# Performance work log

Hardware: AMD Instinct MI355X
Metric: run time of the kernel (lower is better)

The kernel has to match this reference:

```python
import jax, jax.numpy as jnp
import numpy as np

B, N, INNER, OUT, DEPTH = 128, 128, 40, 512, 2
F = INNER + 1  # last channel is the bond/adjacency channel


def setup_inputs() -> dict:
    key = jax.random.key(0)
    k0, k1, k2, k3, k4 = jax.random.split(key, 5)
    return {
        "graph": jax.random.normal(k0, (B, N, N, F), dtype=jnp.float32),
        # build() inits: identity tiled for W_inner, uniform*0.05 for W_output, zero biases.
        # We add small noise so the reference exercises nondegenerate paths.
        "W_inner": jnp.tile(jnp.eye(INNER, dtype=jnp.float32)[None], (DEPTH + 1, 1, 1))
        + 0.05 * jax.random.normal(k1, (DEPTH + 1, INNER, INNER), dtype=jnp.float32),
        "b_inner": 0.05 * jax.random.normal(k2, (DEPTH + 1, 1, INNER), dtype=jnp.float32),
        "W_output": 0.05 * jax.random.normal(k3, (DEPTH + 1, INNER, OUT), dtype=jnp.float32),
        "b_output": 0.05 * jax.random.normal(k4, (DEPTH + 1, 1, OUT), dtype=jnp.float32),
    }


def reference(graph, W_inner, b_inner, W_output, b_output):
    depth = W_inner.shape[0] - 1

    def fp_contrib(attrs, d):
        # softmax over fingerprint dim, summed over atoms -> (OUT,)
        logits = attrs[:, :-1] @ W_output[d] + b_output[d, 0]
        return jax.nn.softmax(logits, axis=-1).sum(axis=0)

    def single(g):  # g: (N, N, F) for one molecule
        n = g.shape[0]
        # attributes[i, f] = g[i, i, f]  (per-atom diagonal extraction)
        attrs = jnp.diagonal(g, axis1=0, axis2=1).T  # (N, F)
        bonds = g[:, :, -1]                          # (N, N)
        boa = bonds + jnp.eye(n, dtype=g.dtype)      # bonds_or_atoms
        fp = fp_contrib(attrs, 0)
        cur = g
        for d in range(1, depth + 1):
            # sum over neighbors j: pre[i, f] = sum_j cur[i, j, f], drop bond channel
            pre = cur[:, :, :-1].sum(axis=1)                     # (N, INNER)
            new_core = pre @ W_inner[d] + b_inner[d, 0]          # linear inner activation
            new_attrs = jnp.concatenate([new_core, attrs[:, -1:]], axis=1)  # (N, F)
            # new_graph[i,j,f] = cur[i,j,f] + boa[j,i] * (new_attrs[i,f] - attrs[i,f])
            cur = cur + boa.T[:, :, None] * (new_attrs - attrs)[:, None, :]
            attrs = new_attrs
            fp = fp + fp_contrib(attrs, d)
        return fp  # (OUT,)

    return jax.vmap(single)(graph)  # (B, OUT)
```

## Files before the change

### kernel.cpp

```cpp
#include <hip/hip_runtime.h>

#define Bn 128
#define Nn 128
#define Fn 41
#define INNERn 40
#define OUTn 512
#define SLAB (Nn*Fn)

__global__ __launch_bounds__(256) void k1_reduce(
    const float* __restrict__ g, float* __restrict__ X0,
    float* __restrict__ pre1, float* __restrict__ S)
{
    __shared__ float lds[SLAB];
    __shared__ float part[6*INNERn];
    const int t = threadIdx.x;
    const int blk = blockIdx.x;
    const int b = blk >> 7;
    const int i = blk & 127;

    if (t < 40) {
        X0[(size_t)blk*INNERn + t] = g[(size_t)blk*SLAB + i*Fn + t];
    }

    const float4* __restrict__ src = (const float4*)(g + (size_t)blk * SLAB);
    float4* dst = (float4*)lds;
    #pragma unroll
    for (int it = 0; it < 5; ++it) dst[t + 256*it] = src[t + 256*it];
    if (t < (SLAB/4 - 1280)) dst[1280 + t] = src[1280 + t];
    __syncthreads();

    if (t < 240) {
        const int grp = t / 40;
        const int f = t - grp*40;
        float s = 0.f;
        #pragma unroll 4
        for (int j = grp; j < Nn; j += 6) s += lds[j*Fn + f];
        part[grp*INNERn + f] = s;
    }
    if (t < 128) {
        float v = lds[t*Fn + 40] + ((t == i) ? 1.f : 0.f);
        atomicAdd(&S[b*Nn + t], v);
    }
    __syncthreads();
    if (t < 40) {
        float s = part[t] + part[INNERn + t] + part[2*INNERn + t]
                + part[3*INNERn + t] + part[4*INNERn + t] + part[5*INNERn + t];
        pre1[(size_t)blk*INNERn + t] = s;
    }
}

__global__ __launch_bounds__(256) void k2_chain(
    const float* __restrict__ pre1, const float* __restrict__ X0,
    const float* __restrict__ S, const float* __restrict__ Wi,
    const float* __restrict__ bi, float* __restrict__ X1, float* __restrict__ X2)
{
    __shared__ float W1[INNERn*INNERn], W2[INNERn*INNERn];
    __shared__ float A[16*INNERn];
    __shared__ float T[16*INNERn];
    __shared__ float Sv[16];
    const int t = threadIdx.x;
    const size_t row0 = (size_t)blockIdx.x * 16;

    for (int idx = t; idx < INNERn*INNERn; idx += 256) {
        W1[idx] = Wi[INNERn*INNERn + idx];
        W2[idx] = Wi[2*INNERn*INNERn + idx];
    }
    for (int idx = t; idx < 16*INNERn; idx += 256) {
        A[idx] = pre1[row0*INNERn + idx];
        T[idx] = X0[row0*INNERn + idx];
    }
    if (t < 16) Sv[t] = S[row0 + t];
    __syncthreads();

    float c1[3];
    #pragma unroll
    for (int p = 0; p < 3; ++p) {
        int idx = t + 256*p;
        if (idx < 16*INNERn) {
            int r = idx / INNERn, c = idx - r*INNERn;
            float acc = bi[INNERn + c];
            #pragma unroll 4
            for (int k = 0; k < INNERn; ++k) acc = fmaf(A[r*INNERn + k], W1[k*INNERn + c], acc);
            c1[p] = acc;
        }
    }
    __syncthreads();
    #pragma unroll
    for (int p = 0; p < 3; ++p) {
        int idx = t + 256*p;
        if (idx < 16*INNERn) {
            int r = idx / INNERn;
            X1[row0*INNERn + idx] = c1[p];
            A[idx] = A[idx] + Sv[r] * (c1[p] - T[idx]);
        }
    }
    __syncthreads();
    #pragma unroll
    for (int p = 0; p < 3; ++p) {
        int idx = t + 256*p;
        if (idx < 16*INNERn) {
            int r = idx / INNERn, c = idx - r*INNERn;
            float acc = bi[2*INNERn + c];
            #pragma unroll 4
            for (int k = 0; k < INNERn; ++k) acc = fmaf(A[r*INNERn + k], W2[k*INNERn + c], acc);
            X2[row0*INNERn + idx] = acc;
        }
    }
}

__global__ __launch_bounds__(256) void k3_softmax(
    const float* __restrict__ X, const float* __restrict__ Wo,
    const float* __restrict__ bo_g, float* __restrict__ out)
{
    __shared__ float lx[32*INNERn];
    __shared__ float lacc4[4*OUTn];
    const int t = threadIdx.x;
    const int lane = t & 63;
    const int w = t >> 6;
    const int bx = blockIdx.x;
    const int d = bx >> 9;
    const int rem = bx & 511;
    const int b = rem >> 2;
    const int chunk = rem & 3;

    const float* __restrict__ Xb = X + (((size_t)d*Bn + b)*Nn + chunk*32)*INNERn;
    for (int idx = t; idx < 32*INNERn; idx += 256) lx[idx] = Xb[idx];
    __syncthreads();

    const float* __restrict__ W = Wo + (size_t)d*INNERn*OUTn + lane*8;
    float acc[8][8];
    #pragma unroll
    for (int r = 0; r < 8; ++r)
        #pragma unroll
        for (int u = 0; u < 8; ++u) acc[r][u] = 0.f;

    for (int k = 0; k < INNERn; ++k) {
        const float4* __restrict__ wp = (const float4*)(W + k*OUTn);
        float4 w0 = wp[0];
        float4 w1 = wp[1];
        float wv[8] = {w0.x, w0.y, w0.z, w0.w, w1.x, w1.y, w1.z, w1.w};
        #pragma unroll
        for (int r = 0; r < 8; ++r) {
            float a = lx[(w*8 + r)*INNERn + k];
            #pragma unroll
            for (int u = 0; u < 8; ++u) acc[r][u] = fmaf(a, wv[u], acc[r][u]);
        }
    }

    const float4* __restrict__ bp = (const float4*)(bo_g + d*OUTn + lane*8);
    float4 b0 = bp[0];
    float4 b1 = bp[1];
    float bv[8] = {b0.x, b0.y, b0.z, b0.w, b1.x, b1.y, b1.z, b1.w};
    float colacc[8];
    #pragma unroll
    for (int u = 0; u < 8; ++u) colacc[u] = 0.f;

    #pragma unroll
    for (int r = 0; r < 8; ++r) {
        float lg[8];
        float m = -3.4e38f;
        #pragma unroll
        for (int u = 0; u < 8; ++u) { lg[u] = acc[r][u] + bv[u]; m = fmaxf(m, lg[u]); }
        #pragma unroll
        for (int off = 32; off > 0; off >>= 1) m = fmaxf(m, __shfl_xor(m, off));
        float s = 0.f, e[8];
        #pragma unroll
        for (int u = 0; u < 8; ++u) { e[u] = __expf(lg[u] - m); s += e[u]; }
        #pragma unroll
        for (int off = 32; off > 0; off >>= 1) s += __shfl_xor(s, off);
        float inv = 1.f / s;
        #pragma unroll
        for (int u = 0; u < 8; ++u) colacc[u] = fmaf(e[u], inv, colacc[u]);
    }

    #pragma unroll
    for (int u = 0; u < 8; ++u) lacc4[w*OUTn + lane*8 + u] = colacc[u];
    __syncthreads();
    for (int idx = t; idx < OUTn; idx += 256) {
        float s = lacc4[idx] + lacc4[OUTn + idx] + lacc4[2*OUTn + idx] + lacc4[3*OUTn + idx];
        atomicAdd(&out[(size_t)b*OUTn + idx], s);
    }
}

extern "C" void kernel_launch(void* const* d_in, const int* in_sizes, int n_in,
                              void* d_out, int out_size, void* d_ws, size_t ws_size,
                              hipStream_t stream) {
    const float* g        = (const float*)d_in[0];
    const float* W_inner  = (const float*)d_in[1];
    const float* b_inner  = (const float*)d_in[2];
    const float* W_output = (const float*)d_in[3];
    const float* b_output = (const float*)d_in[4];
    float* out = (float*)d_out;
    float* ws  = (float*)d_ws;

    const size_t nBN = (size_t)Bn * Nn;
    float* X    = ws;
    float* X0   = X;
    float* X1   = X + nBN * INNERn;
    float* X2   = X + 2 * nBN * INNERn;
    float* pre1 = X + 3 * nBN * INNERn;
    float* S    = pre1 + nBN * INNERn;

    hipMemsetAsync(S, 0, nBN * sizeof(float), stream);
    hipMemsetAsync(d_out, 0, (size_t)out_size * sizeof(float), stream);

    k1_reduce<<<Bn*Nn, 256, 0, stream>>>(g, X0, pre1, S);
    k2_chain<<<(Bn*Nn)/16, 256, 0, stream>>>(pre1, X0, S, W_inner, b_inner, X1, X2);
    k3_softmax<<<3*Bn*4, 256, 0, stream>>>(X, W_output, b_output, out);
}
```

Measured before the change: 507.9 us.

## Use direct global-to-LDS loads, fuse zeroing, and double softmax rows per block

The k1 slab copy now uses global_load_lds builtins, so data goes from global memory into LDS without passing through registers, and X0 is read from LDS instead of being re-read from global memory. The two memsets are replaced by one zeroing kernel. The softmax kernel processes 64 rows per block with 16 rows per wave, which halves the block count and the Wo reloads and atomics per output, at the cost of much higher register pressure (128 accumulators per thread). The direct-to-LDS loads depend on the exact slot layout being correct.

After: 504.3 us. About the same (-0.7%).

```diff
diff --git a/kernel.cpp b/kernel.cpp
--- a/kernel.cpp
+++ b/kernel.cpp
@@ -6,6 +6,12 @@
 #define INNERn 40
 #define OUTn 512
 #define SLAB (Nn*Fn)
+
+__global__ __launch_bounds__(256) void k0_zero(float* __restrict__ S, float* __restrict__ out) {
+    const int idx = blockIdx.x * 256 + threadIdx.x;
+    if (idx < Bn*Nn) S[idx] = 0.f;
+    out[idx] = 0.f;
+}
 
 __global__ __launch_bounds__(256) void k1_reduce(
     const float* __restrict__ g, float* __restrict__ X0,
@@ -14,19 +20,28 @@
     __shared__ float lds[SLAB];
     __shared__ float part[6*INNERn];
     const int t = threadIdx.x;
+    const int lane = t & 63;
+    const int w = t >> 6;
     const int blk = blockIdx.x;
     const int b = blk >> 7;
     const int i = blk & 127;
 
-    if (t < 40) {
-        X0[(size_t)blk*INNERn + t] = g[(size_t)blk*SLAB + i*Fn + t];
-    }
-
-    const float4* __restrict__ src = (const float4*)(g + (size_t)blk * SLAB);
-    float4* dst = (float4*)lds;
-    #pragma unroll
-    for (int it = 0; it < 5; ++it) dst[t + 256*it] = src[t + 256*it];
-    if (t < (SLAB/4 - 1280)) dst[1280 + t] = src[1280 + t];
+    const float* __restrict__ src = g + (size_t)blk * SLAB;
+
+    #pragma unroll
+    for (int it = 0; it < 5; ++it) {
+        const int slotbase = it*256 + w*64;
+        __builtin_amdgcn_global_load_lds(
+            (const __attribute__((address_space(1))) unsigned int*)(src + (size_t)(slotbase + lane)*4),
+            (__attribute__((address_space(3))) unsigned int*)(lds + (size_t)slotbase*4),
+            16, 0, 0);
+    }
+    if (w == 0 && lane < 32) {
+        __builtin_amdgcn_global_load_lds(
+            (const __attribute__((address_space(1))) unsigned int*)(src + (size_t)(1280 + lane)*4),
+            (__attribute__((address_space(3))) unsigned int*)(lds + (size_t)1280*4),
+            16, 0, 0);
+    }
     __syncthreads();
 
     if (t < 240) {
@@ -40,6 +55,9 @@
     if (t < 128) {
         float v = lds[t*Fn + 40] + ((t == i) ? 1.f : 0.f);
         atomicAdd(&S[b*Nn + t], v);
+    }
+    if (t < 40) {
+        X0[(size_t)blk*INNERn + t] = lds[i*Fn + t];
     }
     __syncthreads();
     if (t < 40) {
@@ -108,29 +126,29 @@
     }
 }
 
-__global__ __launch_bounds__(256) void k3_softmax(
+__global__ __launch_bounds__(256, 2) void k3_softmax(
     const float* __restrict__ X, const float* __restrict__ Wo,
     const float* __restrict__ bo_g, float* __restrict__ out)
 {
-    __shared__ float lx[32*INNERn];
+    __shared__ float lx[64*INNERn];
     __shared__ float lacc4[4*OUTn];
     const int t = threadIdx.x;
     const int lane = t & 63;
     const int w = t >> 6;
     const int bx = blockIdx.x;
-    const int d = bx >> 9;
-    const int rem = bx & 511;
-    const int b = rem >> 2;
-    const int chunk = rem & 3;
-
-    const float* __restrict__ Xb = X + (((size_t)d*Bn + b)*Nn + chunk*32)*INNERn;
-    for (int idx = t; idx < 32*INNERn; idx += 256) lx[idx] = Xb[idx];
+    const int d = bx >> 8;
+    const int rem = bx & 255;
+    const int b = rem >> 1;
+    const int chunk = rem & 1;
+
+    const float* __restrict__ Xb = X + (((size_t)d*Bn + b)*Nn + chunk*64)*INNERn;
+    for (int idx = t; idx < 64*INNERn; idx += 256) lx[idx] = Xb[idx];
     __syncthreads();
 
     const float* __restrict__ W = Wo + (size_t)d*INNERn*OUTn + lane*8;
-    float acc[8][8];
-    #pragma unroll
-    for (int r = 0; r < 8; ++r)
+    float acc[16][8];
+    #pragma unroll
+    for (int r = 0; r < 16; ++r)
         #pragma unroll
         for (int u = 0; u < 8; ++u) acc[r][u] = 0.f;
 
@@ -140,8 +158,8 @@
         float4 w1 = wp[1];
         float wv[8] = {w0.x, w0.y, w0.z, w0.w, w1.x, w1.y, w1.z, w1.w};
         #pragma unroll
-        for (int r = 0; r < 8; ++r) {
-            float a = lx[(w*8 + r)*INNERn + k];
+        for (int r = 0; r < 16; ++r) {
+            float a = lx[(w*16 + r)*INNERn + k];
             #pragma unroll
             for (int u = 0; u < 8; ++u) acc[r][u] = fmaf(a, wv[u], acc[r][u]);
         }
@@ -156,7 +174,7 @@
     for (int u = 0; u < 8; ++u) colacc[u] = 0.f;
 
     #pragma unroll
-    for (int r = 0; r < 8; ++r) {
+    for (int r = 0; r < 16; ++r) {
         float lg[8];
         float m = -3.4e38f;
         #pragma unroll
@@ -201,10 +219,8 @@
     float* pre1 = X + 3 * nBN * INNERn;
     float* S    = pre1 + nBN * INNERn;
 
-    hipMemsetAsync(S, 0, nBN * sizeof(float), stream);
-    hipMemsetAsync(d_out, 0, (size_t)out_size * sizeof(float), stream);
-
+    k0_zero<<<256, 256, 0, stream>>>(S, out);
     k1_reduce<<<Bn*Nn, 256, 0, stream>>>(g, X0, pre1, S);
     k2_chain<<<(Bn*Nn)/16, 256, 0, stream>>>(pre1, X0, S, W_inner, b_inner, X1, X2);
-    k3_softmax<<<3*Bn*4, 256, 0, stream>>>(X, W_output, b_output, out);
-}
+    k3_softmax<<<3*Bn*2, 256, 0, stream>>>(X, W_output, b_output, out);
+}
```
